# Performance work log

Hardware: AMD Instinct MI355X
Metric: run time of the kernel (lower is better)

The kernel has to match this reference:

```python
import jax, jax.numpy as jnp
import numpy as np

V, H, L, B = 50257, 1024, 10, 256

def setup_inputs() -> dict:
    key = jax.random.key(0)
    ks = jax.random.split(key, 16)
    s = 0.02
    return {
        "tokens": jax.random.randint(ks[0], (1, B), 0, V),
        "hidden": jax.random.normal(ks[1], (1, B, H), jnp.float32),
        "encoder_outputs": jax.random.normal(ks[2], (L, H), jnp.float32),
        "emb": jax.random.normal(ks[3], (V, H), jnp.float32) * s,
        "attn_W": jax.random.normal(ks[4], (L, 2 * H), jnp.float32) * s,
        "attn_b": jnp.zeros((L,), jnp.float32),
        "comb_W": jax.random.normal(ks[5], (H, 2 * H), jnp.float32) * s,
        "comb_b": jnp.zeros((H,), jnp.float32),
        "W_ih": jax.random.normal(ks[6], (3 * H, H), jnp.float32) * s,
        "W_hh": jax.random.normal(ks[7], (3 * H, H), jnp.float32) * s,
        "b_ih": jnp.zeros((3 * H,), jnp.float32),
        "b_hh": jnp.zeros((3 * H,), jnp.float32),
        "out_W": jax.random.normal(ks[8], (V, H), jnp.float32) * s,
        "out_b": jnp.zeros((V,), jnp.float32),
    }

def reference(tokens, hidden, encoder_outputs, emb, attn_W, attn_b, comb_W, comb_b,
              W_ih, W_hh, b_ih, b_hh, out_W, out_b):
    # Embedding lookup (dropout = identity, eval mode)
    embedded = emb[tokens[0]]            # [B, H]
    h = hidden[-1]                       # [B, H]
    # Attention over encoder outputs
    attn_logits = jnp.concatenate([embedded, h], axis=1) @ attn_W.T + attn_b
    attn_weights = jax.nn.softmax(attn_logits, axis=1)          # [B, L]
    attn_applied = attn_weights @ encoder_outputs                # [B, H]
    # Combine + relu -> GRU input
    x = jnp.concatenate([embedded, attn_applied], axis=1) @ comb_W.T + comb_b
    x = jax.nn.relu(x)                   # [B, H]
    # Single GRU step (PyTorch gate ordering: r, z, n)
    gi = x @ W_ih.T + b_ih               # [B, 3H]
    gh = h @ W_hh.T + b_hh               # [B, 3H]
    i_r, i_z, i_n = jnp.split(gi, 3, axis=1)
    h_r, h_z, h_n = jnp.split(gh, 3, axis=1)
    r = jax.nn.sigmoid(i_r + h_r)
    z = jax.nn.sigmoid(i_z + h_z)
    n = jnp.tanh(i_n + r * h_n)
    h_new = (1.0 - z) * n + z * h        # [B, H]
    # Output projection + log_softmax
    output = jax.nn.log_softmax(h_new @ out_W.T + out_b, axis=1)  # [B, V]
    return (output, h_new[None], attn_weights)
```

## Files before the change

### kernel.cpp

```cpp
#include <hip/hip_runtime.h>
#include <math.h>
#include <stdint.h>

#define B_SZ 256
#define H_SZ 1024
#define L_SZ 10
#define V_SZ 50257

typedef __attribute__((ext_vector_type(8))) short short8;
typedef __attribute__((ext_vector_type(4))) float floatx4;

__device__ __forceinline__ unsigned f2bf_bits(float f) {
    unsigned u = __float_as_uint(f);
    return (u + 0x7FFFu + ((u >> 16) & 1u)) >> 16;
}

__device__ __forceinline__ short8 cvt8(float4 a, float4 b) {
    unsigned r0, r1, r2, r3;
    asm("v_cvt_pk_bf16_f32 %0, %1, %2" : "=v"(r0) : "v"(a.x), "v"(a.y));
    asm("v_cvt_pk_bf16_f32 %0, %1, %2" : "=v"(r1) : "v"(a.z), "v"(a.w));
    asm("v_cvt_pk_bf16_f32 %0, %1, %2" : "=v"(r2) : "v"(b.x), "v"(b.y));
    asm("v_cvt_pk_bf16_f32 %0, %1, %2" : "=v"(r3) : "v"(b.z), "v"(b.w));
    union { unsigned u[4]; short8 s; } u;
    u.u[0] = r0; u.u[1] = r1; u.u[2] = r2; u.u[3] = r3;
    return u.s;
}

template<int MSUB, int NF, int RELU, int PD, int ABF>
__global__ __launch_bounds__(256) void gemm_direct(
    const void* __restrict__ A, const float* __restrict__ W,
    const float* __restrict__ bias, float* __restrict__ Cf,
    short* __restrict__ C16, int N, int K)
{
    const int tid  = threadIdx.x;
    const int wave = tid >> 6;
    const int lane = tid & 63;
    const int quad = lane >> 4;
    const int l16  = lane & 15;

    const int n0 = blockIdx.x * (NF * 16);
    const int m_base = blockIdx.y * (MSUB * 64) + wave * (MSUB * 16);
    const int nc = K >> 5;

    const float* wp[NF];
#pragma unroll
    for (int nf = 0; nf < NF; ++nf) {
        int r = n0 + nf * 16 + l16;
        if (r >= N) r = N - 1;
        wp[nf] = W + (size_t)r * K + quad * 8;
    }
    const short* ab[MSUB];
    const float* af[MSUB];
#pragma unroll
    for (int ms = 0; ms < MSUB; ++ms) {
        int r = m_base + ms * 16 + l16;
        if (ABF) ab[ms] = (const short*)A + (size_t)r * K + quad * 8;
        else     af[ms] = (const float*)A + (size_t)r * K + quad * 8;
    }

    floatx4 zero = {0.f, 0.f, 0.f, 0.f};
    floatx4 acc[MSUB][NF];
#pragma unroll
    for (int ms = 0; ms < MSUB; ++ms)
#pragma unroll
        for (int nf = 0; nf < NF; ++nf) acc[ms][nf] = zero;

    float4 sw[PD][NF][2];
    short8 sa[PD][MSUB];
    float4 sf[PD][MSUB][2];

    auto lstage = [&](int p, int c) {
#pragma unroll
        for (int nf = 0; nf < NF; ++nf) {
            sw[p][nf][0] = *(const float4*)(wp[nf] + (size_t)c * 32);
            sw[p][nf][1] = *(const float4*)(wp[nf] + (size_t)c * 32 + 4);
        }
#pragma unroll
        for (int ms = 0; ms < MSUB; ++ms) {
            if constexpr (ABF) {
                sa[p][ms] = *(const short8*)(ab[ms] + (size_t)c * 32);
            } else {
                sf[p][ms][0] = *(const float4*)(af[ms] + (size_t)c * 32);
                sf[p][ms][1] = *(const float4*)(af[ms] + (size_t)c * 32 + 4);
            }
        }
    };
    auto compute = [&](int p) {
        short8 bfr[NF];
#pragma unroll
        for (int nf = 0; nf < NF; ++nf)
            bfr[nf] = cvt8(sw[p][nf][0], sw[p][nf][1]);
#pragma unroll
        for (int ms = 0; ms < MSUB; ++ms) {
            short8 afr;
            if constexpr (ABF) afr = sa[p][ms];
            else               afr = cvt8(sf[p][ms][0], sf[p][ms][1]);
#pragma unroll
            for (int nf = 0; nf < NF; ++nf)
                acc[ms][nf] = __builtin_amdgcn_mfma_f32_16x16x32_bf16(
                    afr, bfr[nf], acc[ms][nf], 0, 0, 0);
        }
    };

#pragma unroll
    for (int p = 0; p < PD; ++p) lstage(p, p);

    for (int cb = 0; cb < nc - PD; cb += PD) {
#pragma unroll
        for (int p = 0; p < PD; ++p) {
            compute(p);
            lstage(p, cb + p + PD);
        }
    }
#pragma unroll
    for (int p = 0; p < PD; ++p) compute(p);

    float bia[NF];
#pragma unroll
    for (int nf = 0; nf < NF; ++nf) {
        int n = n0 + nf * 16 + l16;
        bia[nf] = (n < N) ? bias[n] : 0.f;
    }
#pragma unroll
    for (int ms = 0; ms < MSUB; ++ms) {
        int mb = m_base + ms * 16 + quad * 4;
#pragma unroll
        for (int nf = 0; nf < NF; ++nf) {
            int n = n0 + nf * 16 + l16;
            if (n < N) {
#pragma unroll
                for (int i = 0; i < 4; ++i) {
                    float v = acc[ms][nf][i] + bia[nf];
                    if (RELU) v = fmaxf(v, 0.f);
                    if (Cf)  Cf[(size_t)(mb + i) * N + n] = v;
                    if (C16) C16[(size_t)(mb + i) * N + n] = (short)f2bf_bits(v);
                }
            }
        }
    }
}

template<int MSUB, int NF, int RELU, int PD, int ABF>
__global__ __launch_bounds__(256) void gemm_direct_dual(
    const void* __restrict__ A0, const float* __restrict__ W0,
    const float* __restrict__ b0, float* __restrict__ C0,
    const void* __restrict__ A1, const float* __restrict__ W1,
    const float* __restrict__ b1, float* __restrict__ C1,
    int N, int K)
{
    const void*  A = blockIdx.z ? A1 : A0;
    const float* W = blockIdx.z ? W1 : W0;
    const float* b = blockIdx.z ? b1 : b0;
    float*       C = blockIdx.z ? C1 : C0;

    const int tid  = threadIdx.x;
    const int wave = tid >> 6;
    const int lane = tid & 63;
    const int quad = lane >> 4;
    const int l16  = lane & 15;
    const int n0 = blockIdx.x * (NF * 16);
    const int m_base = blockIdx.y * (MSUB * 64) + wave * (MSUB * 16);
    const int nc = K >> 5;

    const float* wp[NF];
#pragma unroll
    for (int nf = 0; nf < NF; ++nf) {
        int r = n0 + nf * 16 + l16;
        if (r >= N) r = N - 1;
        wp[nf] = W + (size_t)r * K + quad * 8;
    }
    const short* ab[MSUB];
    const float* af[MSUB];
#pragma unroll
    for (int ms = 0; ms < MSUB; ++ms) {
        int r = m_base + ms * 16 + l16;
        if (ABF) ab[ms] = (const short*)A + (size_t)r * K + quad * 8;
        else     af[ms] = (const float*)A + (size_t)r * K + quad * 8;
    }

    floatx4 zero = {0.f, 0.f, 0.f, 0.f};
    floatx4 acc[MSUB][NF];
#pragma unroll
    for (int ms = 0; ms < MSUB; ++ms)
#pragma unroll
        for (int nf = 0; nf < NF; ++nf) acc[ms][nf] = zero;

    float4 sw[PD][NF][2];
    short8 sa[PD][MSUB];
    float4 sf[PD][MSUB][2];

    auto lstage = [&](int p, int c) {
#pragma unroll
        for (int nf = 0; nf < NF; ++nf) {
            sw[p][nf][0] = *(const float4*)(wp[nf] + (size_t)c * 32);
            sw[p][nf][1] = *(const float4*)(wp[nf] + (size_t)c * 32 + 4);
        }
#pragma unroll
        for (int ms = 0; ms < MSUB; ++ms) {
            if constexpr (ABF) {
                sa[p][ms] = *(const short8*)(ab[ms] + (size_t)c * 32);
            } else {
                sf[p][ms][0] = *(const float4*)(af[ms] + (size_t)c * 32);
                sf[p][ms][1] = *(const float4*)(af[ms] + (size_t)c * 32 + 4);
            }
        }
    };
    auto compute = [&](int p) {
        short8 bfr[NF];
#pragma unroll
        for (int nf = 0; nf < NF; ++nf)
            bfr[nf] = cvt8(sw[p][nf][0], sw[p][nf][1]);
#pragma unroll
        for (int ms = 0; ms < MSUB; ++ms) {
            short8 afr;
            if constexpr (ABF) afr = sa[p][ms];
            else               afr = cvt8(sf[p][ms][0], sf[p][ms][1]);
#pragma unroll
            for (int nf = 0; nf < NF; ++nf)
                acc[ms][nf] = __builtin_amdgcn_mfma_f32_16x16x32_bf16(
                    afr, bfr[nf], acc[ms][nf], 0, 0, 0);
        }
    };

#pragma unroll
    for (int p = 0; p < PD; ++p) lstage(p, p);
    for (int cb = 0; cb < nc - PD; cb += PD) {
#pragma unroll
        for (int p = 0; p < PD; ++p) { compute(p); lstage(p, cb + p + PD); }
    }
#pragma unroll
    for (int p = 0; p < PD; ++p) compute(p);

    float bia[NF];
#pragma unroll
    for (int nf = 0; nf < NF; ++nf) {
        int n = n0 + nf * 16 + l16;
        bia[nf] = (n < N) ? b[n] : 0.f;
    }
#pragma unroll
    for (int ms = 0; ms < MSUB; ++ms) {
        int mb = m_base + ms * 16 + quad * 4;
#pragma unroll
        for (int nf = 0; nf < NF; ++nf) {
            int n = n0 + nf * 16 + l16;
            if (n < N) {
#pragma unroll
                for (int i = 0; i < 4; ++i)
                    C[(size_t)(mb + i) * N + n] = acc[ms][nf][i] + bia[nf];
            }
        }
    }
}

__global__ __launch_bounds__(256) void attn_kernel(
    const int* __restrict__ tokens, const float* __restrict__ hidden,
    const float* __restrict__ enc, const float* __restrict__ emb,
    const float* __restrict__ attn_W, const float* __restrict__ attn_b,
    float* __restrict__ catf, short* __restrict__ cat16,
    short* __restrict__ h16, float* __restrict__ attn_w_out)
{
    const int b = blockIdx.x;
    const int tid = threadIdx.x;
    const int tok = tokens[b];
    const float* erow = emb + (size_t)tok * H_SZ;
    const float* hrow = hidden + (size_t)b * H_SZ;

    __shared__ float red[L_SZ][256];
    __shared__ float wts[L_SZ];

    float acc[L_SZ];
#pragma unroll
    for (int l = 0; l < L_SZ; ++l) acc[l] = 0.f;

    for (int i = tid; i < H_SZ; i += 256) {
        float e = erow[i];
        float hv = hrow[i];
        if (catf)  catf[(size_t)b * 2 * H_SZ + i] = e;
        if (cat16) cat16[(size_t)b * 2 * H_SZ + i] = (short)f2bf_bits(e);
        if (h16)   h16[(size_t)b * H_SZ + i] = (short)f2bf_bits(hv);
#pragma unroll
        for (int l = 0; l < L_SZ; ++l) {
            acc[l] += e * attn_W[l * 2 * H_SZ + i] + hv * attn_W[l * 2 * H_SZ + H_SZ + i];
        }
    }
#pragma unroll
    for (int l = 0; l < L_SZ; ++l) red[l][tid] = acc[l];
    __syncthreads();
    for (int s = 128; s > 0; s >>= 1) {
        if (tid < s) {
#pragma unroll
            for (int l = 0; l < L_SZ; ++l) red[l][tid] += red[l][tid + s];
        }
        __syncthreads();
    }
    if (tid == 0) {
        float m = -INFINITY;
        float lg[L_SZ];
#pragma unroll
        for (int l = 0; l < L_SZ; ++l) {
            lg[l] = red[l][0] + attn_b[l];
            m = fmaxf(m, lg[l]);
        }
        float s = 0.f;
#pragma unroll
        for (int l = 0; l < L_SZ; ++l) {
            float e = expf(lg[l] - m);
            wts[l] = e;
            s += e;
        }
        float inv = 1.f / s;
#pragma unroll
        for (int l = 0; l < L_SZ; ++l) {
            wts[l] *= inv;
            attn_w_out[(size_t)b * L_SZ + l] = wts[l];
        }
    }
    __syncthreads();

    for (int i = tid; i < H_SZ; i += 256) {
        float s = 0.f;
#pragma unroll
        for (int l = 0; l < L_SZ; ++l) s += wts[l] * enc[l * H_SZ + i];
        if (catf)  catf[(size_t)b * 2 * H_SZ + H_SZ + i] = s;
        if (cat16) cat16[(size_t)b * 2 * H_SZ + H_SZ + i] = (short)f2bf_bits(s);
    }
}

__global__ __launch_bounds__(256) void gru_combine(
    const float* __restrict__ gi, const float* __restrict__ gh,
    const float* __restrict__ hidden, float* __restrict__ h_new,
    short* __restrict__ hb16)
{
    int idx = blockIdx.x * blockDim.x + threadIdx.x;
    if (idx >= B_SZ * H_SZ) return;
    int b = idx >> 10;
    int j = idx & (H_SZ - 1);
    const float* gib = gi + (size_t)b * 3 * H_SZ;
    const float* ghb = gh + (size_t)b * 3 * H_SZ;
    float i_r = gib[j], i_z = gib[H_SZ + j], i_n = gib[2 * H_SZ + j];
    float h_r = ghb[j], h_z = ghb[H_SZ + j], h_n = ghb[2 * H_SZ + j];
    float r = 1.f / (1.f + expf(-(i_r + h_r)));
    float z = 1.f / (1.f + expf(-(i_z + h_z)));
    float n = tanhf(i_n + r * h_n);
    float h = hidden[idx];
    float hn = (1.f - z) * n + z * h;
    h_new[idx] = hn;
    if (hb16) hb16[idx] = (short)f2bf_bits(hn);
}

__global__ __launch_bounds__(1024) void logsoftmax_v3(float* __restrict__ out)
{
    const int b = blockIdx.x;
    float* row = out + (size_t)b * V_SZ;
    const int tid = threadIdx.x;
    const int wave = tid >> 6;
    const int lane = tid & 63;

    const int head = (int)(((16u - ((uintptr_t)row & 15u)) & 15u) >> 2);
    const int nv = (V_SZ - head) >> 2;
    const float4* r4 = (const float4*)(row + head);
    const int tail_start = head + (nv << 2);

    float m = -INFINITY, s = 0.f;
    if (tid < head) {
        float v = row[tid];
        m = v; s = 1.f;
    }
    int i = tid;
    for (; i + 3072 < nv; i += 4096) {
        float4 v0 = r4[i], v1 = r4[i + 1024], v2 = r4[i + 2048], v3 = r4[i + 3072];
        float m0 = fmaxf(fmaxf(v0.x, v0.y), fmaxf(v0.z, v0.w));
        float m1 = fmaxf(fmaxf(v1.x, v1.y), fmaxf(v1.z, v1.w));
        float m2 = fmaxf(fmaxf(v2.x, v2.y), fmaxf(v2.z, v2.w));
        float m3 = fmaxf(fmaxf(v3.x, v3.y), fmaxf(v3.z, v3.w));
        float mv = fmaxf(fmaxf(m0, m1), fmaxf(m2, m3));
        if (mv > m) { s *= expf(m - mv); m = mv; }
        s += expf(v0.x - m) + expf(v0.y - m) + expf(v0.z - m) + expf(v0.w - m);
        s += expf(v1.x - m) + expf(v1.y - m) + expf(v1.z - m) + expf(v1.w - m);
        s += expf(v2.x - m) + expf(v2.y - m) + expf(v2.z - m) + expf(v2.w - m);
        s += expf(v3.x - m) + expf(v3.y - m) + expf(v3.z - m) + expf(v3.w - m);
    }
    for (; i < nv; i += 1024) {
        float4 v = r4[i];
        float mv = fmaxf(fmaxf(v.x, v.y), fmaxf(v.z, v.w));
        if (mv > m) { s *= expf(m - mv); m = mv; }
        s += expf(v.x - m) + expf(v.y - m) + expf(v.z - m) + expf(v.w - m);
    }
    for (int t = tail_start + tid; t < V_SZ; t += 1024) {
        float v = row[t];
        if (v > m) { s *= expf(m - v); m = v; }
        s += expf(v - m);
    }

    for (int off = 32; off > 0; off >>= 1) {
        float m2 = __shfl_down(m, off);
        float s2 = __shfl_down(s, off);
        float mn = fmaxf(m, m2);
        s = s * expf(m - mn) + s2 * expf(m2 - mn);
        m = mn;
    }
    __shared__ float smax[16], ssum[16], slse;
    if (lane == 0) { smax[wave] = m; ssum[wave] = s; }
    __syncthreads();
    if (tid == 0) {
        float M = smax[0], S = ssum[0];
        for (int w = 1; w < 16; ++w) {
            float mn = fmaxf(M, smax[w]);
            S = S * expf(M - mn) + ssum[w] * expf(smax[w] - mn);
            M = mn;
        }
        slse = M + logf(S);
    }
    __syncthreads();
    const float lse = slse;

    if (tid < head) row[tid] -= lse;
    float4* w4 = (float4*)(row + head);
    i = tid;
    for (; i + 3072 < nv; i += 4096) {
        float4 v0 = r4[i], v1 = r4[i + 1024], v2 = r4[i + 2048], v3 = r4[i + 3072];
        v0.x -= lse; v0.y -= lse; v0.z -= lse; v0.w -= lse;
        v1.x -= lse; v1.y -= lse; v1.z -= lse; v1.w -= lse;
        v2.x -= lse; v2.y -= lse; v2.z -= lse; v2.w -= lse;
        v3.x -= lse; v3.y -= lse; v3.z -= lse; v3.w -= lse;
        w4[i] = v0; w4[i + 1024] = v1; w4[i + 2048] = v2; w4[i + 3072] = v3;
    }
    for (; i < nv; i += 1024) {
        float4 v = r4[i];
        v.x -= lse; v.y -= lse; v.z -= lse; v.w -= lse;
        w4[i] = v;
    }
    for (int t = tail_start + tid; t < V_SZ; t += 1024) row[t] -= lse;
}

extern "C" void kernel_launch(void* const* d_in, const int* in_sizes, int n_in,
                              void* d_out, int out_size, void* d_ws, size_t ws_size,
                              hipStream_t stream)
{
    const int*   tokens = (const int*)d_in[0];
    const float* hidden = (const float*)d_in[1];
    const float* enc    = (const float*)d_in[2];
    const float* emb    = (const float*)d_in[3];
    const float* attn_W = (const float*)d_in[4];
    const float* attn_b = (const float*)d_in[5];
    const float* comb_W = (const float*)d_in[6];
    const float* comb_b = (const float*)d_in[7];
    const float* W_ih   = (const float*)d_in[8];
    const float* W_hh   = (const float*)d_in[9];
    const float* b_ih   = (const float*)d_in[10];
    const float* b_hh   = (const float*)d_in[11];
    const float* out_W  = (const float*)d_in[12];
    const float* out_b  = (const float*)d_in[13];

    float* out = (float*)d_out;
    float* logits     = out;
    float* h_new      = out + (size_t)B_SZ * V_SZ;
    float* attn_w_out = h_new + (size_t)B_SZ * H_SZ;

    const size_t need = (size_t)B_SZ * 5 * H_SZ * sizeof(short)
                      + (size_t)B_SZ * 6 * H_SZ * sizeof(float);
    const bool use_ws = (d_ws != nullptr) && (ws_size >= need);

    if (use_ws) {
        short* cat16 = (short*)d_ws;
        short* x16   = cat16 + (size_t)B_SZ * 2 * H_SZ;
        short* hin16 = x16   + (size_t)B_SZ * H_SZ;
        short* hb16  = hin16 + (size_t)B_SZ * H_SZ;
        float* gi    = (float*)(hb16 + (size_t)B_SZ * H_SZ);
        float* gh    = gi + (size_t)B_SZ * 3 * H_SZ;

        attn_kernel<<<B_SZ, 256, 0, stream>>>(tokens, hidden, enc, emb, attn_W,
                                              attn_b, nullptr, cat16, hin16,
                                              attn_w_out);
        gemm_direct<1, 2, 1, 4, 1><<<dim3(H_SZ / 32, 4), 256, 0, stream>>>(
            cat16, comb_W, comb_b, nullptr, x16, H_SZ, 2 * H_SZ);
        gemm_direct_dual<1, 2, 0, 4, 1><<<dim3(3 * H_SZ / 32, 4, 2), 256, 0, stream>>>(
            x16, W_ih, b_ih, gi, hin16, W_hh, b_hh, gh, 3 * H_SZ, H_SZ);
        gru_combine<<<(B_SZ * H_SZ + 255) / 256, 256, 0, stream>>>(
            gi, gh, hidden, h_new, hb16);
        gemm_direct<4, 4, 0, 2, 1><<<dim3((V_SZ + 63) / 64, 1), 256, 0, stream>>>(
            hb16, out_W, out_b, logits, nullptr, V_SZ, H_SZ);
    } else {
        float* cat = logits;
        float* x   = cat + (size_t)B_SZ * 2 * H_SZ;
        float* gi  = x   + (size_t)B_SZ * H_SZ;
        float* gh  = gi  + (size_t)B_SZ * 3 * H_SZ;

        attn_kernel<<<B_SZ, 256, 0, stream>>>(tokens, hidden, enc, emb, attn_W,
                                              attn_b, cat, nullptr, nullptr,
                                              attn_w_out);
        gemm_direct<1, 2, 1, 4, 0><<<dim3(H_SZ / 32, 4), 256, 0, stream>>>(
            cat, comb_W, comb_b, x, nullptr, H_SZ, 2 * H_SZ);
        gemm_direct_dual<1, 2, 0, 4, 0><<<dim3(3 * H_SZ / 32, 4, 2), 256, 0, stream>>>(
            x, W_ih, b_ih, gi, hidden, W_hh, b_hh, gh, 3 * H_SZ, H_SZ);
        gru_combine<<<(B_SZ * H_SZ + 255) / 256, 256, 0, stream>>>(
            gi, gh, hidden, h_new, nullptr);
        gemm_direct<4, 4, 0, 2, 0><<<dim3((V_SZ + 63) / 64, 1), 256, 0, stream>>>(
            h_new, out_W, out_b, logits, nullptr, V_SZ, H_SZ);
    }
    logsoftmax_v3<<<B_SZ, 1024, 0, stream>>>(logits);
}
```

Measured before the change: 656.3 us.

## Stage full-K weight panels in swizzled LDS as bf16 and vectorize attention

GEMM kernels now load each block's whole weight panel (rows × full K) once, convert it to bf16, and store it in XOR-swizzled shared memory. The MFMA loop then reads B fragments from LDS while streaming A from global with double buffering. Before, every wave reloaded and reconverted fp32 weights from global. The output projection uses 32-row panels with 4 waves × 64 batch rows, so out_W is read once and converted once per element, at the cost of a larger LDS footprint and lower occupancy. The attention kernel is also vectorized to float4 loads and packed bf16 stores.

```diff
diff --git a/kernel.cpp b/kernel.cpp
--- a/kernel.cpp
+++ b/kernel.cpp
@@ -26,37 +26,61 @@
     return u.s;
 }
 
-template<int MSUB, int NF, int RELU, int PD, int ABF>
-__global__ __launch_bounds__(256) void gemm_direct(
+__device__ __forceinline__ uint2 pk4(float4 v) {
+    uint2 r;
+    asm("v_cvt_pk_bf16_f32 %0, %1, %2" : "=v"(r.x) : "v"(v.x), "v"(v.y));
+    asm("v_cvt_pk_bf16_f32 %0, %1, %2" : "=v"(r.y) : "v"(v.z), "v"(v.w));
+    return r;
+}
+
+template<int MSUB, int NF, int KK, int RELU, int ABF>
+__device__ __forceinline__ void panel_body(
+    short* lds,
     const void* __restrict__ A, const float* __restrict__ W,
     const float* __restrict__ bias, float* __restrict__ Cf,
-    short* __restrict__ C16, int N, int K)
-{
+    short* __restrict__ C16, int N)
+{
+    constexpr int PROWS = NF * 16;
+    constexpr int NC = KK / 32;
+
     const int tid  = threadIdx.x;
     const int wave = tid >> 6;
     const int lane = tid & 63;
     const int quad = lane >> 4;
     const int l16  = lane & 15;
 
-    const int n0 = blockIdx.x * (NF * 16);
+    const int n0 = blockIdx.x * PROWS;
     const int m_base = blockIdx.y * (MSUB * 64) + wave * (MSUB * 16);
-    const int nc = K >> 5;
-
-    const float* wp[NF];
-#pragma unroll
-    for (int nf = 0; nf < NF; ++nf) {
-        int r = n0 + nf * 16 + l16;
-        if (r >= N) r = N - 1;
-        wp[nf] = W + (size_t)r * K + quad * 8;
-    }
+
+    constexpr int ITERS = PROWS * KK / 2048;
+#pragma unroll
+    for (int it = 0; it < ITERS; ++it) {
+        int e   = it * 2048 + tid * 8;
+        int row = e / KK;
+        int k   = e % KK;
+        int gr  = n0 + row;
+        if (gr >= N) gr = N - 1;
+        const float* src = W + (size_t)gr * KK + k;
+        float4 a0 = *(const float4*)src;
+        float4 a1 = *(const float4*)(src + 4);
+        int pb = row * (KK * 2) + ((k * 2) ^ ((row & 7) << 4));
+        *(short8*)((char*)lds + pb) = cvt8(a0, a1);
+    }
+    __syncthreads();
+
     const short* ab[MSUB];
     const float* af[MSUB];
 #pragma unroll
     for (int ms = 0; ms < MSUB; ++ms) {
         int r = m_base + ms * 16 + l16;
-        if (ABF) ab[ms] = (const short*)A + (size_t)r * K + quad * 8;
-        else     af[ms] = (const float*)A + (size_t)r * K + quad * 8;
-    }
+        if (ABF) ab[ms] = (const short*)A + (size_t)r * KK + quad * 8;
+        else     af[ms] = (const float*)A + (size_t)r * KK + quad * 8;
+    }
+
+    int rb[NF];
+#pragma unroll
+    for (int nf = 0; nf < NF; ++nf) rb[nf] = (nf * 16 + l16) * (KK * 2);
+    const int r7x = (l16 & 7) << 4;
 
     floatx4 zero = {0.f, 0.f, 0.f, 0.f};
     floatx4 acc[MSUB][NF];
@@ -65,55 +89,48 @@
 #pragma unroll
         for (int nf = 0; nf < NF; ++nf) acc[ms][nf] = zero;
 
-    float4 sw[PD][NF][2];
-    short8 sa[PD][MSUB];
-    float4 sf[PD][MSUB][2];
-
-    auto lstage = [&](int p, int c) {
-#pragma unroll
-        for (int nf = 0; nf < NF; ++nf) {
-            sw[p][nf][0] = *(const float4*)(wp[nf] + (size_t)c * 32);
-            sw[p][nf][1] = *(const float4*)(wp[nf] + (size_t)c * 32 + 4);
-        }
+    auto loadA = [&](short8* s, int c) {
 #pragma unroll
         for (int ms = 0; ms < MSUB; ++ms) {
             if constexpr (ABF) {
-                sa[p][ms] = *(const short8*)(ab[ms] + (size_t)c * 32);
+                s[ms] = *(const short8*)(ab[ms] + c * 32);
             } else {
-                sf[p][ms][0] = *(const float4*)(af[ms] + (size_t)c * 32);
-                sf[p][ms][1] = *(const float4*)(af[ms] + (size_t)c * 32 + 4);
+                float4 a0 = *(const float4*)(af[ms] + c * 32);
+                float4 a1 = *(const float4*)(af[ms] + c * 32 + 4);
+                s[ms] = cvt8(a0, a1);
             }
         }
     };
-    auto compute = [&](int p) {
+    auto comp = [&](const short8* s, int c) {
         short8 bfr[NF];
 #pragma unroll
-        for (int nf = 0; nf < NF; ++nf)
-            bfr[nf] = cvt8(sw[p][nf][0], sw[p][nf][1]);
-#pragma unroll
-        for (int ms = 0; ms < MSUB; ++ms) {
-            short8 afr;
-            if constexpr (ABF) afr = sa[p][ms];
-            else               afr = cvt8(sf[p][ms][0], sf[p][ms][1]);
+        for (int nf = 0; nf < NF; ++nf) {
+            int kb = (c * 64 + quad * 16) ^ r7x;
+            bfr[nf] = *(const short8*)((char*)lds + rb[nf] + kb);
+        }
+#pragma unroll
+        for (int ms = 0; ms < MSUB; ++ms)
 #pragma unroll
             for (int nf = 0; nf < NF; ++nf)
                 acc[ms][nf] = __builtin_amdgcn_mfma_f32_16x16x32_bf16(
-                    afr, bfr[nf], acc[ms][nf], 0, 0, 0);
-        }
+                    s[ms], bfr[nf], acc[ms][nf], 0, 0, 0);
     };
 
-#pragma unroll
-    for (int p = 0; p < PD; ++p) lstage(p, p);
-
-    for (int cb = 0; cb < nc - PD; cb += PD) {
-#pragma unroll
-        for (int p = 0; p < PD; ++p) {
-            compute(p);
-            lstage(p, cb + p + PD);
-        }
-    }
-#pragma unroll
-    for (int p = 0; p < PD; ++p) compute(p);
+    short8 s0[MSUB], s1[MSUB];
+    loadA(s0, 0);
+    loadA(s1, 1);
+#pragma unroll
+    for (int cc = 0; cc < NC; cc += 2) {
+        short8 n0s[MSUB], n1s[MSUB];
+        if (cc + 2 < NC) loadA(n0s, cc + 2);
+        if (cc + 3 < NC) loadA(n1s, cc + 3);
+        comp(s0, cc);
+        comp(s1, cc + 1);
+        if (cc + 2 < NC) {
+#pragma unroll
+            for (int ms = 0; ms < MSUB; ++ms) { s0[ms] = n0s[ms]; s1[ms] = n1s[ms]; }
+        }
+    }
 
     float bia[NF];
 #pragma unroll
@@ -140,116 +157,29 @@
     }
 }
 
-template<int MSUB, int NF, int RELU, int PD, int ABF>
-__global__ __launch_bounds__(256) void gemm_direct_dual(
+template<int MSUB, int NF, int KK, int RELU, int ABF>
+__global__ __launch_bounds__(256) void gemm_panel(
+    const void* __restrict__ A, const float* __restrict__ W,
+    const float* __restrict__ bias, float* __restrict__ Cf,
+    short* __restrict__ C16, int N)
+{
+    __shared__ __align__(16) short lds[NF * 16 * KK];
+    panel_body<MSUB, NF, KK, RELU, ABF>(lds, A, W, bias, Cf, C16, N);
+}
+
+template<int MSUB, int NF, int KK, int ABF>
+__global__ __launch_bounds__(256) void gemm_panel_dual(
     const void* __restrict__ A0, const float* __restrict__ W0,
     const float* __restrict__ b0, float* __restrict__ C0,
     const void* __restrict__ A1, const float* __restrict__ W1,
-    const float* __restrict__ b1, float* __restrict__ C1,
-    int N, int K)
-{
+    const float* __restrict__ b1, float* __restrict__ C1, int N)
+{
+    __shared__ __align__(16) short lds[NF * 16 * KK];
     const void*  A = blockIdx.z ? A1 : A0;
     const float* W = blockIdx.z ? W1 : W0;
     const float* b = blockIdx.z ? b1 : b0;
     float*       C = blockIdx.z ? C1 : C0;
-
-    const int tid  = threadIdx.x;
-    const int wave = tid >> 6;
-    const int lane = tid & 63;
-    const int quad = lane >> 4;
-    const int l16  = lane & 15;
-    const int n0 = blockIdx.x * (NF * 16);
-    const int m_base = blockIdx.y * (MSUB * 64) + wave * (MSUB * 16);
-    const int nc = K >> 5;
-
-    const float* wp[NF];
-#pragma unroll
-    for (int nf = 0; nf < NF; ++nf) {
-        int r = n0 + nf * 16 + l16;
-        if (r >= N) r = N - 1;
-        wp[nf] = W + (size_t)r * K + quad * 8;
-    }
-    const short* ab[MSUB];
-    const float* af[MSUB];
-#pragma unroll
-    for (int ms = 0; ms < MSUB; ++ms) {
-        int r = m_base + ms * 16 + l16;
-        if (ABF) ab[ms] = (const short*)A + (size_t)r * K + quad * 8;
-        else     af[ms] = (const float*)A + (size_t)r * K + quad * 8;
-    }
-
-    floatx4 zero = {0.f, 0.f, 0.f, 0.f};
-    floatx4 acc[MSUB][NF];
-#pragma unroll
-    for (int ms = 0; ms < MSUB; ++ms)
-#pragma unroll
-        for (int nf = 0; nf < NF; ++nf) acc[ms][nf] = zero;
-
-    float4 sw[PD][NF][2];
-    short8 sa[PD][MSUB];
-    float4 sf[PD][MSUB][2];
-
-    auto lstage = [&](int p, int c) {
-#pragma unroll
-        for (int nf = 0; nf < NF; ++nf) {
-            sw[p][nf][0] = *(const float4*)(wp[nf] + (size_t)c * 32);
-            sw[p][nf][1] = *(const float4*)(wp[nf] + (size_t)c * 32 + 4);
-        }
-#pragma unroll
-        for (int ms = 0; ms < MSUB; ++ms) {
-            if constexpr (ABF) {
-                sa[p][ms] = *(const short8*)(ab[ms] + (size_t)c * 32);
-            } else {
-                sf[p][ms][0] = *(const float4*)(af[ms] + (size_t)c * 32);
-                sf[p][ms][1] = *(const float4*)(af[ms] + (size_t)c * 32 + 4);
-            }
-        }
-    };
-    auto compute = [&](int p) {
-        short8 bfr[NF];
-#pragma unroll
-        for (int nf = 0; nf < NF; ++nf)
-            bfr[nf] = cvt8(sw[p][nf][0], sw[p][nf][1]);
-#pragma unroll
-        for (int ms = 0; ms < MSUB; ++ms) {
-            short8 afr;
-            if constexpr (ABF) afr = sa[p][ms];
-            else               afr = cvt8(sf[p][ms][0], sf[p][ms][1]);
-#pragma unroll
-            for (int nf = 0; nf < NF; ++nf)
-                acc[ms][nf] = __builtin_amdgcn_mfma_f32_16x16x32_bf16(
-                    afr, bfr[nf], acc[ms][nf], 0, 0, 0);
-        }
-    };
-
-#pragma unroll
-    for (int p = 0; p < PD; ++p) lstage(p, p);
-    for (int cb = 0; cb < nc - PD; cb += PD) {
-#pragma unroll
-        for (int p = 0; p < PD; ++p) { compute(p); lstage(p, cb + p + PD); }
-    }
-#pragma unroll
-    for (int p = 0; p < PD; ++p) compute(p);
-
-    float bia[NF];
-#pragma unroll
-    for (int nf = 0; nf < NF; ++nf) {
-        int n = n0 + nf * 16 + l16;
-        bia[nf] = (n < N) ? b[n] : 0.f;
-    }
-#pragma unroll
-    for (int ms = 0; ms < MSUB; ++ms) {
-        int mb = m_base + ms * 16 + quad * 4;
-#pragma unroll
-        for (int nf = 0; nf < NF; ++nf) {
-            int n = n0 + nf * 16 + l16;
-            if (n < N) {
-#pragma unroll
-                for (int i = 0; i < 4; ++i)
-                    C[(size_t)(mb + i) * N + n] = acc[ms][nf][i] + bia[nf];
-            }
-        }
-    }
+    panel_body<MSUB, NF, KK, 0, ABF>(lds, A, W, b, C, nullptr, N);
 }
 
 __global__ __launch_bounds__(256) void attn_kernel(
@@ -259,30 +189,31 @@
     float* __restrict__ catf, short* __restrict__ cat16,
     short* __restrict__ h16, float* __restrict__ attn_w_out)
 {
-    const int b = blockIdx.x;
+    const int b   = blockIdx.x;
     const int tid = threadIdx.x;
     const int tok = tokens[b];
-    const float* erow = emb + (size_t)tok * H_SZ;
-    const float* hrow = hidden + (size_t)b * H_SZ;
+
+    const float4* e4 = (const float4*)(emb + (size_t)tok * H_SZ);
+    const float4* h4 = (const float4*)(hidden + (size_t)b * H_SZ);
+    const float4* w4 = (const float4*)attn_W;
+    float4 e = e4[tid];
+    float4 h = h4[tid];
+
+    if (catf)  ((float4*)(catf + (size_t)b * 2 * H_SZ))[tid] = e;
+    if (cat16) ((uint2*)(cat16 + (size_t)b * 2 * H_SZ))[tid] = pk4(e);
+    if (h16)   ((uint2*)(h16 + (size_t)b * H_SZ))[tid] = pk4(h);
+
+    float acc[L_SZ];
+#pragma unroll
+    for (int l = 0; l < L_SZ; ++l) {
+        float4 we = w4[l * 512 + tid];
+        float4 wh = w4[l * 512 + 256 + tid];
+        acc[l] = e.x * we.x + e.y * we.y + e.z * we.z + e.w * we.w
+               + h.x * wh.x + h.y * wh.y + h.z * wh.z + h.w * wh.w;
+    }
 
     __shared__ float red[L_SZ][256];
     __shared__ float wts[L_SZ];
-
-    float acc[L_SZ];
-#pragma unroll
-    for (int l = 0; l < L_SZ; ++l) acc[l] = 0.f;
-
-    for (int i = tid; i < H_SZ; i += 256) {
-        float e = erow[i];
-        float hv = hrow[i];
-        if (catf)  catf[(size_t)b * 2 * H_SZ + i] = e;
-        if (cat16) cat16[(size_t)b * 2 * H_SZ + i] = (short)f2bf_bits(e);
-        if (h16)   h16[(size_t)b * H_SZ + i] = (short)f2bf_bits(hv);
-#pragma unroll
-        for (int l = 0; l < L_SZ; ++l) {
-            acc[l] += e * attn_W[l * 2 * H_SZ + i] + hv * attn_W[l * 2 * H_SZ + H_SZ + i];
-        }
-    }
 #pragma unroll
     for (int l = 0; l < L_SZ; ++l) red[l][tid] = acc[l];
     __syncthreads();
@@ -304,9 +235,9 @@
         float s = 0.f;
 #pragma unroll
         for (int l = 0; l < L_SZ; ++l) {
-            float e = expf(lg[l] - m);
-            wts[l] = e;
-            s += e;
+            float ev = expf(lg[l] - m);
+            wts[l] = ev;
+            s += ev;
         }
         float inv = 1.f / s;
 #pragma unroll
@@ -317,13 +248,15 @@
     }
     __syncthreads();
 
-    for (int i = tid; i < H_SZ; i += 256) {
-        float s = 0.f;
-#pragma unroll
-        for (int l = 0; l < L_SZ; ++l) s += wts[l] * enc[l * H_SZ + i];
-        if (catf)  catf[(size_t)b * 2 * H_SZ + H_SZ + i] = s;
-        if (cat16) cat16[(size_t)b * 2 * H_SZ + H_SZ + i] = (short)f2bf_bits(s);
-    }
+    float4 s = {0.f, 0.f, 0.f, 0.f};
+#pragma unroll
+    for (int l = 0; l < L_SZ; ++l) {
+        float4 ev = ((const float4*)enc)[l * 256 + tid];
+        float wv = wts[l];
+        s.x += wv * ev.x; s.y += wv * ev.y; s.z += wv * ev.z; s.w += wv * ev.w;
+    }
+    if (catf)  ((float4*)(catf + (size_t)b * 2 * H_SZ + H_SZ))[tid] = s;
+    if (cat16) ((uint2*)(cat16 + (size_t)b * 2 * H_SZ + H_SZ))[tid] = pk4(s);
 }
 
 __global__ __launch_bounds__(256) void gru_combine(
@@ -457,6 +390,8 @@
     float* h_new      = out + (size_t)B_SZ * V_SZ;
     float* attn_w_out = h_new + (size_t)B_SZ * H_SZ;
 
+    const int NPANEL = (V_SZ + 31) / 32;
+
     const size_t need = (size_t)B_SZ * 5 * H_SZ * sizeof(short)
                       + (size_t)B_SZ * 6 * H_SZ * sizeof(float);
     const bool use_ws = (d_ws != nullptr) && (ws_size >= need);
@@ -472,14 +407,14 @@
         attn_kernel<<<B_SZ, 256, 0, stream>>>(tokens, hidden, enc, emb, attn_W,
                                               attn_b, nullptr, cat16, hin16,
                                               attn_w_out);
-        gemm_direct<1, 2, 1, 4, 1><<<dim3(H_SZ / 32, 4), 256, 0, stream>>>(
-            cat16, comb_W, comb_b, nullptr, x16, H_SZ, 2 * H_SZ);
-        gemm_direct_dual<1, 2, 0, 4, 1><<<dim3(3 * H_SZ / 32, 4, 2), 256, 0, stream>>>(
-            x16, W_ih, b_ih, gi, hin16, W_hh, b_hh, gh, 3 * H_SZ, H_SZ);
+        gemm_panel<1, 1, 2048, 1, 1><<<dim3(H_SZ / 16, 4), 256, 0, stream>>>(
+            cat16, comb_W, comb_b, nullptr, x16, H_SZ);
+        gemm_panel_dual<1, 2, 1024, 1><<<dim3(3 * H_SZ / 32, 4, 2), 256, 0, stream>>>(
+            x16, W_ih, b_ih, gi, hin16, W_hh, b_hh, gh, 3 * H_SZ);
         gru_combine<<<(B_SZ * H_SZ + 255) / 256, 256, 0, stream>>>(
             gi, gh, hidden, h_new, hb16);
-        gemm_direct<4, 4, 0, 2, 1><<<dim3((V_SZ + 63) / 64, 1), 256, 0, stream>>>(
-            hb16, out_W, out_b, logits, nullptr, V_SZ, H_SZ);
+        gemm_panel<4, 2, 1024, 0, 1><<<dim3(NPANEL, 1), 256, 0, stream>>>(
+            hb16, out_W, out_b, logits, nullptr, V_SZ);
     } else {
         float* cat = logits;
         float* x   = cat + (size_t)B_SZ * 2 * H_SZ;
@@ -489,14 +424,14 @@
         attn_kernel<<<B_SZ, 256, 0, stream>>>(tokens, hidden, enc, emb, attn_W,
                                               attn_b, cat, nullptr, nullptr,
                                               attn_w_out);
-        gemm_direct<1, 2, 1, 4, 0><<<dim3(H_SZ / 32, 4), 256, 0, stream>>>(
-            cat, comb_W, comb_b, x, nullptr, H_SZ, 2 * H_SZ);
-        gemm_direct_dual<1, 2, 0, 4, 0><<<dim3(3 * H_SZ / 32, 4, 2), 256, 0, stream>>>(
-            x, W_ih, b_ih, gi, hidden, W_hh, b_hh, gh, 3 * H_SZ, H_SZ);
+        gemm_panel<1, 1, 2048, 1, 0><<<dim3(H_SZ / 16, 4), 256, 0, stream>>>(
+            cat, comb_W, comb_b, x, nullptr, H_SZ);
+        gemm_panel_dual<1, 2, 1024, 0><<<dim3(3 * H_SZ / 32, 4, 2), 256, 0, stream>>>(
+            x, W_ih, b_ih, gi, hidden, W_hh, b_hh, gh, 3 * H_SZ);
         gru_combine<<<(B_SZ * H_SZ + 255) / 256, 256, 0, stream>>>(
             gi, gh, hidden, h_new, nullptr);
-        gemm_direct<4, 4, 0, 2, 0><<<dim3((V_SZ + 63) / 64, 1), 256, 0, stream>>>(
-            h_new, out_W, out_b, logits, nullptr, V_SZ, H_SZ);
+        gemm_panel<4, 2, 1024, 0, 0><<<dim3(NPANEL, 1), 256, 0, stream>>>(
+            h_new, out_W, out_b, logits, nullptr, V_SZ);
     }
     logsoftmax_v3<<<B_SZ, 1024, 0, stream>>>(logits);
 }
```

Result: faster. 588.8 us (-10.3%).
